# Kernel optimization log

Hardware: AMD Instinct MI355X
Metric: run time of the kernel (lower is better)

The kernel has to match this reference:

```python
import jax, jax.numpy as jnp
import numpy as np

N = 65536       # num nodes
F = 128         # num_features
D = 256         # embedding_dim
E = N * 8       # num edges
CS = 32         # target_cluster_size
DEPTH = 8
H = 8
NCLS = 10


def setup_inputs() -> dict:
    key = jax.random.key(0)
    ks = jax.random.split(key, 16)
    r = lambda k, shp: (jax.random.normal(k, shp, jnp.float32) * 0.02)
    return {
        "x": jax.random.normal(ks[0], (N, F), jnp.float32),
        "edge_index": jax.random.randint(ks[1], (2, E), 0, N),
        "W_in": r(ks[2], (F, D)), "b_in": jnp.zeros((D,), jnp.float32),
        "W_gat": r(ks[3], (D, D)), "a_src": r(ks[4], (D,)), "a_dst": r(ks[5], (D,)),
        "b_gat": jnp.zeros((D,), jnp.float32),
        "W_emb": r(ks[6], (CS * D, D)), "b_emb": jnp.zeros((D,), jnp.float32),
        "class_tok": r(ks[7], (D,)),
        "ln1_s": jnp.ones((DEPTH, D), jnp.float32), "ln1_b": jnp.zeros((DEPTH, D), jnp.float32),
        "Wqkv": r(ks[8], (DEPTH, D, 3 * D)), "bqkv": jnp.zeros((DEPTH, 3 * D), jnp.float32),
        "Wproj": r(ks[9], (DEPTH, D, D)), "bproj": jnp.zeros((DEPTH, D), jnp.float32),
        "ln2_s": jnp.ones((DEPTH, D), jnp.float32), "ln2_b": jnp.zeros((DEPTH, D), jnp.float32),
        "W1": r(ks[10], (DEPTH, D, 4 * D)), "b1": jnp.zeros((DEPTH, 4 * D), jnp.float32),
        "W2": r(ks[11], (DEPTH, 4 * D, D)), "b2": jnp.zeros((DEPTH, D), jnp.float32),
        "W_cls": r(ks[12], (D, NCLS)), "b_cls": jnp.zeros((NCLS,), jnp.float32),
    }


def _layernorm(x, s, b):
    m = jnp.mean(x, -1, keepdims=True)
    v = jnp.var(x, -1, keepdims=True)
    return (x - m) * jax.lax.rsqrt(v + 1e-5) * s + b


def _forward(x, edge_index, W_in, b_in, W_gat, a_src, a_dst, b_gat, W_emb, b_emb,
             class_tok, ln1_s, ln1_b, Wqkv, bqkv, Wproj, bproj, ln2_s, ln2_b,
             W1, b1, W2, b2, W_cls, b_cls):
    # input_layer: LazyLinear(F -> D)
    h = x @ W_in + b_in                                   # [N, D]
    # GATConv(D -> D), 1 head, add_self_loops=True
    loop = jnp.arange(N)
    src = jnp.concatenate([edge_index[0], loop])          # message source j
    dst = jnp.concatenate([edge_index[1], loop])          # message target i
    Wh = h @ W_gat                                        # [N, D]
    e = jax.nn.leaky_relu((Wh @ a_src)[src] + (Wh @ a_dst)[dst], 0.2)
    emax = jax.ops.segment_max(e, dst, num_segments=N)
    ee = jnp.exp(e - emax[dst])
    denom = jax.ops.segment_sum(ee, dst, num_segments=N)
    alpha = ee / denom[dst]                               # softmax over incoming edges
    h = jax.ops.segment_sum(alpha[:, None] * Wh[src], dst, num_segments=N) + b_gat
    # clusters of 32 contiguous nodes: gather, flatten, embeddings_layer (32*D -> D)
    tok = h.reshape(N // CS, CS * D) @ W_emb + b_emb      # [num_clusters, D]
    seq = jnp.concatenate([class_tok[None, :], tok])[None]  # [1, S, D], S = num_clusters + 1
    scale = (D // H) ** -0.5
    for i in range(DEPTH):
        y = _layernorm(seq, ln1_s[i], ln1_b[i])
        qkv = (y @ Wqkv[i] + bqkv[i]).reshape(1, -1, 3, H, D // H)
        q, k, v = qkv[:, :, 0], qkv[:, :, 1], qkv[:, :, 2]
        att = jax.nn.softmax(jnp.einsum('bshd,bthd->bhst', q, k) * scale, axis=-1)
        o = jnp.einsum('bhst,bthd->bshd', att, v).reshape(1, -1, D)
        seq = seq + (o @ Wproj[i] + bproj[i])
        y = _layernorm(seq, ln2_s[i], ln2_b[i])
        seq = seq + (jax.nn.gelu(y @ W1[i] + b1[i], approximate=False) @ W2[i] + b2[i])
    # to_class on the class token
    return seq[0, 0][None, :] @ W_cls + b_cls             # [1, NCLS]


def reference(x, edge_index, W_in, b_in, W_gat, a_src, a_dst, b_gat, W_emb, b_emb,
              class_tok, ln1_s, ln1_b, Wqkv, bqkv, Wproj, bproj, ln2_s, ln2_b,
              W1, b1, W2, b2, W_cls, b_cls):
    return _forward(x, edge_index, W_in, b_in, W_gat, a_src, a_dst, b_gat, W_emb,
                    b_emb, class_tok, ln1_s, ln1_b, Wqkv, bqkv, Wproj, bproj,
                    ln2_s, ln2_b, W1, b1, W2, b2, W_cls, b_cls)
```

## Files before the change

### kernel.cpp

```cpp
#include <hip/hip_runtime.h>
#include <math.h>

#define N_NODES 65536
#define F_IN 128
#define D_MODEL 256
#define E_EDGES 524288
#define EE_EDGES 589824
#define SEQ_LEN 2049
#define SEQ_PAD 2112
#define NHEAD 8
#define HDIM 32
#define NCLS 10
#define NSPLIT 4

typedef unsigned short u16;
typedef __attribute__((ext_vector_type(8))) short s8v;
typedef __attribute__((ext_vector_type(4))) float f4v;

__device__ __forceinline__ u16 f2bf(float f)
{
    union { float f; unsigned u; } v; v.f = f;
    unsigned r = v.u + 0x7FFF + ((v.u >> 16) & 1);
    return (u16)(r >> 16);
}
__device__ __forceinline__ float bf2f(u16 h)
{
    union { unsigned u; float f; } v; v.u = ((unsigned)h) << 16;
    return v.f;
}

__global__ __launch_bounds__(256) void prep_weight(
    const float* __restrict__ W, u16* __restrict__ Oh, u16* __restrict__ Ol,
    int K, int N, long long strideW, long long strideO, int write_lo)
{
    const float* Wz = W + (size_t)blockIdx.z * strideW;
    u16* Ohz = Oh + (size_t)blockIdx.z * strideO;
    u16* Olz = Ol + (size_t)blockIdx.z * strideO;
    __shared__ u16 th[64][68];
    __shared__ u16 tl[64][68];
    int kb = blockIdx.x * 64, nb = blockIdx.y * 64;
    int t = threadIdx.x;
    int kr = t >> 4, nc = (t & 15) * 4;
#pragma unroll
    for (int i = 0; i < 4; ++i) {
        int k = kr + i * 16;
        float4 v = *(const float4*)(Wz + (size_t)(kb + k) * N + nb + nc);
        float vv[4] = {v.x, v.y, v.z, v.w};
#pragma unroll
        for (int e = 0; e < 4; ++e) {
            u16 h = f2bf(vv[e]);
            th[k][nc + e] = h;
            if (write_lo) tl[k][nc + e] = f2bf(vv[e] - bf2f(h));
        }
    }
    __syncthreads();
    int nr = t >> 4, kc = (t & 15) * 4;
#pragma unroll
    for (int i = 0; i < 4; ++i) {
        int n = nr + i * 16;
        uint2 oh;
        oh.x = (unsigned)th[kc + 0][n] | ((unsigned)th[kc + 1][n] << 16);
        oh.y = (unsigned)th[kc + 2][n] | ((unsigned)th[kc + 3][n] << 16);
        *(uint2*)(Ohz + (size_t)(nb + n) * K + kb + kc) = oh;
        if (write_lo) {
            uint2 ol;
            ol.x = (unsigned)tl[kc + 0][n] | ((unsigned)tl[kc + 1][n] << 16);
            ol.y = (unsigned)tl[kc + 2][n] | ((unsigned)tl[kc + 3][n] << 16);
            *(uint2*)(Olz + (size_t)(nb + n) * K + kb + kc) = ol;
        }
    }
}

template<int ACT, int RES, int ATOM, int OB, int APRE, int TERMS, int FATT>
__global__ __launch_bounds__(256) void hgemm(
    const void* __restrict__ A, const u16* __restrict__ Al2,
    const u16* __restrict__ Bh, const u16* __restrict__ Bl,
    const float* __restrict__ bias, const float* __restrict__ Rsd,
    float* __restrict__ C, const float* __restrict__ Mp,
    const float* __restrict__ Lp,
    int M, int N, int K, int Kc)
{
    __shared__ __align__(16) u16 SS[(TERMS == 3 ? 4 : 2) * 2048];
    u16* const AhS = SS;
    u16* const BhS = SS + 2048;
    u16* const AlS = SS + 4096;
    u16* const BlS = SS + 6144;
    const int tid = threadIdx.x;
    const int bn = blockIdx.x * 64, bm = blockIdx.y * 64;
    const int kb = blockIdx.z * Kc;
    const int r = tid >> 2, cch = tid & 3;
    const int widx = r * 32 + ((cch ^ ((r >> 1) & 3)) << 3);
    const int w = tid >> 6, lane = tid & 63;
    const int wm = w >> 1, wn = w & 1;
    const int lr = lane & 15, lc = lane >> 4;
    const int ar0 = wm * 32 + lr, ar1 = ar0 + 16;
    const int nr0 = wn * 32 + lr, nr1 = nr0 + 16;
    const int ai0 = ar0 * 32 + ((lc ^ ((ar0 >> 1) & 3)) << 3);
    const int ai1 = ar1 * 32 + ((lc ^ ((ar1 >> 1) & 3)) << 3);
    const int bi0 = nr0 * 32 + ((lc ^ ((nr0 >> 1) & 3)) << 3);
    const int bi1 = nr1 * 32 + ((lc ^ ((nr1 >> 1) & 3)) << 3);

    f4v acc00 = {0.f, 0.f, 0.f, 0.f}, acc01 = acc00, acc10 = acc00, acc11 = acc00;

    const int gr = bm + r;
    const float* apf = (const float*)A + (size_t)gr * K + kb + cch * 8;
    const u16*   aph = (const u16*)A + (size_t)gr * K + kb + cch * 8;
    const u16*   apl = Al2 ? Al2 + (size_t)gr * K + kb + cch * 8 : (const u16*)0;
    const u16* bhp = Bh + (size_t)(bn + r) * K + kb + cch * 8;
    const u16* blp = (TERMS == 3) ? Bl + (size_t)(bn + r) * K + kb + cch * 8
                                  : (const u16*)0;

    float fac_s[FATT ? NSPLIT : 1][FATT ? 2 : 1];
    float invL[FATT ? 2 : 1];
    if (FATT) {
        if (gr < M) {
#pragma unroll
            for (int hh = 0; hh < 2; ++hh) {
                int h = (kb >> 5) + hh;
                float ms[NSPLIT], ls[NSPLIT], Mx = -1e30f;
#pragma unroll
                for (int s = 0; s < NSPLIT; ++s) {
                    ms[s] = Mp[((size_t)s * SEQ_PAD + gr) * NHEAD + h];
                    ls[s] = Lp[((size_t)s * SEQ_PAD + gr) * NHEAD + h];
                    Mx = fmaxf(Mx, ms[s]);
                }
                float L = 0.f;
#pragma unroll
                for (int s = 0; s < NSPLIT; ++s) {
                    float f = __expf(ms[s] - Mx);
                    fac_s[s][hh] = f;
                    L += ls[s] * f;
                }
                invL[hh] = 1.f / L;
            }
        } else {
#pragma unroll
            for (int hh = 0; hh < 2; ++hh) {
                invL[hh] = 0.f;
#pragma unroll
                for (int s = 0; s < NSPLIT; ++s) fac_s[s][hh] = 0.f;
            }
        }
    }

    for (int k0 = 0; k0 < Kc; k0 += 32) {
        s8v hv = {0, 0, 0, 0, 0, 0, 0, 0}, lv = hv;
        if (FATT) {
            if (gr < M) {
                int hh = k0 >> 5;
                float v[8] = {0.f, 0.f, 0.f, 0.f, 0.f, 0.f, 0.f, 0.f};
#pragma unroll
                for (int s = 0; s < NSPLIT; ++s) {
                    const float* op = (const float*)A
                        + ((size_t)s * SEQ_PAD + gr) * 256 + kb + k0 + cch * 8;
                    float4 x0 = *(const float4*)op;
                    float4 x1 = *(const float4*)(op + 4);
                    float f = fac_s[s][hh];
                    v[0] += f * x0.x; v[1] += f * x0.y;
                    v[2] += f * x0.z; v[3] += f * x0.w;
                    v[4] += f * x1.x; v[5] += f * x1.y;
                    v[6] += f * x1.z; v[7] += f * x1.w;
                }
                float il = invL[hh];
#pragma unroll
                for (int e = 0; e < 8; ++e) hv[e] = (short)f2bf(v[e] * il);
            }
        } else if (APRE) {
            if (gr < M) {
                hv = *(const s8v*)aph;
                if (TERMS == 3) lv = *(const s8v*)apl;
            }
        } else {
            float v[8] = {0.f, 0.f, 0.f, 0.f, 0.f, 0.f, 0.f, 0.f};
            if (gr < M) {
                float4 x0 = *(const float4*)apf;
                float4 x1 = *(const float4*)(apf + 4);
                v[0] = x0.x; v[1] = x0.y; v[2] = x0.z; v[3] = x0.w;
                v[4] = x1.x; v[5] = x1.y; v[6] = x1.z; v[7] = x1.w;
            }
#pragma unroll
            for (int e = 0; e < 8; ++e) {
                u16 h = f2bf(v[e]);
                hv[e] = (short)h;
                if (TERMS == 3) lv[e] = (short)f2bf(v[e] - bf2f(h));
            }
        }
        *(s8v*)&AhS[widx] = hv;
        *(s8v*)&BhS[widx] = *(const s8v*)bhp;
        if (TERMS == 3) {
            *(s8v*)&AlS[widx] = lv;
            *(s8v*)&BlS[widx] = *(const s8v*)blp;
        }
        __syncthreads();

        s8v a0h = *(s8v*)&AhS[ai0], a1h = *(s8v*)&AhS[ai1];
        s8v b0h = *(s8v*)&BhS[bi0], b1h = *(s8v*)&BhS[bi1];
        acc00 = __builtin_amdgcn_mfma_f32_16x16x32_bf16(a0h, b0h, acc00, 0, 0, 0);
        acc01 = __builtin_amdgcn_mfma_f32_16x16x32_bf16(a0h, b1h, acc01, 0, 0, 0);
        acc10 = __builtin_amdgcn_mfma_f32_16x16x32_bf16(a1h, b0h, acc10, 0, 0, 0);
        acc11 = __builtin_amdgcn_mfma_f32_16x16x32_bf16(a1h, b1h, acc11, 0, 0, 0);
        if (TERMS == 3) {
            s8v a0l = *(s8v*)&AlS[ai0], a1l = *(s8v*)&AlS[ai1];
            s8v b0l = *(s8v*)&BlS[bi0], b1l = *(s8v*)&BlS[bi1];
            acc00 = __builtin_amdgcn_mfma_f32_16x16x32_bf16(a0h, b0l, acc00, 0, 0, 0);
            acc00 = __builtin_amdgcn_mfma_f32_16x16x32_bf16(a0l, b0h, acc00, 0, 0, 0);
            acc01 = __builtin_amdgcn_mfma_f32_16x16x32_bf16(a0h, b1l, acc01, 0, 0, 0);
            acc01 = __builtin_amdgcn_mfma_f32_16x16x32_bf16(a0l, b1h, acc01, 0, 0, 0);
            acc10 = __builtin_amdgcn_mfma_f32_16x16x32_bf16(a1h, b0l, acc10, 0, 0, 0);
            acc10 = __builtin_amdgcn_mfma_f32_16x16x32_bf16(a1l, b0h, acc10, 0, 0, 0);
            acc11 = __builtin_amdgcn_mfma_f32_16x16x32_bf16(a1h, b1l, acc11, 0, 0, 0);
            acc11 = __builtin_amdgcn_mfma_f32_16x16x32_bf16(a1l, b1h, acc11, 0, 0, 0);
        }
        __syncthreads();
        apf += 32; aph += 32; if (TERMS == 3) apl += 32;
        bhp += 32; if (TERMS == 3) blp += 32;
    }

#pragma unroll
    for (int fg = 0; fg < 4; ++fg) {
        int f = fg >> 1, g = fg & 1;
        f4v a = (fg == 0) ? acc00 : (fg == 1) ? acc01 : (fg == 2) ? acc10 : acc11;
        int col = bn + wn * 32 + g * 16 + lr;
        int row0 = bm + wm * 32 + f * 16 + lc * 4;
#pragma unroll
        for (int j = 0; j < 4; ++j) {
            int rr = row0 + j;
            if (rr < M) {
                float vv = a[j];
                if (ATOM) {
                    atomicAdd(&C[(size_t)rr * N + col], vv);
                } else {
                    if (bias) vv += bias[col];
                    if (ACT == 1) vv = 0.5f * vv * (1.0f + erff(vv * 0.70710678118654752f));
                    if (RES) vv += Rsd[(size_t)rr * N + col];
                    if (OB == 1) ((u16*)C)[(size_t)rr * N + col] = f2bf(vv);
                    else         C[(size_t)rr * N + col] = vv;
                }
            }
        }
    }
}

__global__ void init_seq(float* __restrict__ seq, const float* __restrict__ bias,
                         const float* __restrict__ cls)
{
    int row = blockIdx.x;
    int t = threadIdx.x;
    seq[(size_t)row * 256 + t] = (row == 0) ? cls[t] : bias[t];
}

__global__ void pad_zero_u32(unsigned* __restrict__ p, int n)
{
    int i = blockIdx.x * 256 + threadIdx.x;
    if (i < n) p[i] = 0u;
}

__global__ void vecmat256(const float* __restrict__ v, const float* __restrict__ W,
                          float* __restrict__ out)
{
    int n = threadIdx.x;
    float acc = 0.f;
    for (int k = 0; k < 256; ++k) acc += v[k] * W[k * 256 + n];
    out[n] = acc;
}

__global__ void gat_init(float* __restrict__ emax, float* __restrict__ denom,
                         int* __restrict__ deg)
{
    int i = blockIdx.x * 256 + threadIdx.x;
    emax[i] = -1e30f;
    denom[i] = 0.f;
    deg[i] = 0;
}

__global__ __launch_bounds__(256) void gat_scores(
    const u16* __restrict__ WH, const float* __restrict__ a_src,
    const float* __restrict__ a_dst, float* __restrict__ s_src,
    float* __restrict__ s_dst)
{
    int gid = blockIdx.x * 256 + threadIdx.x;
    int node = gid >> 6;
    int lane = gid & 63;
    uint2 rv = *(const uint2*)(WH + (size_t)node * D_MODEL + (lane << 2));
    float d0 = __uint_as_float(rv.x << 16);
    float d1 = __uint_as_float(rv.x & 0xffff0000u);
    float d2 = __uint_as_float(rv.y << 16);
    float d3 = __uint_as_float(rv.y & 0xffff0000u);
    float4 asv = *(const float4*)(a_src + (lane << 2));
    float4 adv = *(const float4*)(a_dst + (lane << 2));
    float as = d0 * asv.x + d1 * asv.y + d2 * asv.z + d3 * asv.w;
    float ad = d0 * adv.x + d1 * adv.y + d2 * adv.z + d3 * adv.w;
#pragma unroll
    for (int off = 32; off; off >>= 1) {
        as += __shfl_down(as, off);
        ad += __shfl_down(ad, off);
    }
    if (lane == 0) { s_src[node] = as; s_dst[node] = ad; }
}

__device__ __forceinline__ void atomicMaxFloat(float* addr, float val)
{
    int* ai = (int*)addr;
    int old = __float_as_int(*addr);
    while (__int_as_float(old) < val) {
        int prev = atomicCAS(ai, old, __float_as_int(val));
        if (prev == old) break;
        old = prev;
    }
}

__global__ void edge_pass1(const int* __restrict__ ei, const float* __restrict__ s_src,
                           const float* __restrict__ s_dst, float* __restrict__ e_buf,
                           float* __restrict__ emax, int* __restrict__ deg)
{
    int j = blockIdx.x * 256 + threadIdx.x;
    if (j >= EE_EDGES) return;
    int s, d;
    if (j < E_EDGES) { s = ei[j]; d = ei[E_EDGES + j]; }
    else { s = d = j - E_EDGES; }
    float e = s_src[s] + s_dst[d];
    e = (e > 0.f) ? e : 0.2f * e;
    e_buf[j] = e;
    atomicMaxFloat(&emax[d], e);
    atomicAdd(&deg[d], 1);
}

__global__ void scan1(const int* __restrict__ in, int* __restrict__ out_excl,
                      int* __restrict__ bsum)
{
    __shared__ int s[256];
    int t = threadIdx.x;
    int i = blockIdx.x * 256 + t;
    int v = in[i];
    s[t] = v;
    __syncthreads();
    for (int off = 1; off < 256; off <<= 1) {
        int u = (t >= off) ? s[t - off] : 0;
        __syncthreads();
        s[t] += u;
        __syncthreads();
    }
    out_excl[i] = s[t] - v;
    if (t == 255) bsum[blockIdx.x] = s[255];
}

__global__ void scan2(int* __restrict__ bsum)
{
    __shared__ int s[256];
    int t = threadIdx.x;
    int v = bsum[t];
    s[t] = v;
    __syncthreads();
    for (int off = 1; off < 256; off <<= 1) {
        int u = (t >= off) ? s[t - off] : 0;
        __syncthreads();
        s[t] += u;
        __syncthreads();
    }
    bsum[t] = s[t] - v;
}

__global__ void scan3(int* __restrict__ offs, const int* __restrict__ bsum,
                      int* __restrict__ cur)
{
    int i = blockIdx.x * 256 + threadIdx.x;
    int v = offs[i] + bsum[blockIdx.x];
    offs[i] = v;
    cur[i] = v;
}

__global__ void edge_pass2(const int* __restrict__ ei, const float* __restrict__ e_buf,
                           const float* __restrict__ emax, float* __restrict__ denom,
                           int* __restrict__ cur, int* __restrict__ csr_src,
                           float* __restrict__ csr_w)
{
    int j = blockIdx.x * 256 + threadIdx.x;
    if (j >= EE_EDGES) return;
    int s, d;
    if (j < E_EDGES) { s = ei[j]; d = ei[E_EDGES + j]; }
    else { s = d = j - E_EDGES; }
    float ee = __expf(e_buf[j] - emax[d]);
    atomicAdd(&denom[d], ee);
    int pos = atomicAdd(&cur[d], 1);
    csr_src[pos] = s;
    csr_w[pos] = ee;
}

__global__ __launch_bounds__(256) void gat_aggregate(
    const u16* __restrict__ WH, const int* __restrict__ csr_src,
    const float* __restrict__ csr_w, const int* __restrict__ offs,
    const int* __restrict__ deg, const float* __restrict__ denom,
    const float* __restrict__ b_gat, u16* __restrict__ hH)
{
    int gid = blockIdx.x * 256 + threadIdx.x;
    int node = gid >> 6;
    int lane = gid & 63;
    float inv = 1.0f / denom[node];
    float a0 = 0.f, a1 = 0.f, a2 = 0.f, a3 = 0.f;
    int s0 = offs[node], e0 = s0 + deg[node];
    for (int k = s0; k < e0; ++k) {
        int src = csr_src[k];
        float alpha = csr_w[k] * inv;
        uint2 rv = *(const uint2*)(WH + (size_t)src * D_MODEL + (lane << 2));
        a0 += alpha * __uint_as_float(rv.x << 16);
        a1 += alpha * __uint_as_float(rv.x & 0xffff0000u);
        a2 += alpha * __uint_as_float(rv.y << 16);
        a3 += alpha * __uint_as_float(rv.y & 0xffff0000u);
    }
    float4 bg = *(const float4*)(b_gat + (lane << 2));
    float v0 = a0 + bg.x, v1 = a1 + bg.y, v2 = a2 + bg.z, v3 = a3 + bg.w;
    uint2 ho;
    ho.x = (unsigned)f2bf(v0) | ((unsigned)f2bf(v1) << 16);
    ho.y = (unsigned)f2bf(v2) | ((unsigned)f2bf(v3) << 16);
    *(uint2*)(hH + (size_t)node * D_MODEL + (lane << 2)) = ho;
}

__global__ __launch_bounds__(256) void ln_kernel(
    float* __restrict__ seqio, const float* __restrict__ sc,
    const float* __restrict__ bi, u16* __restrict__ Yh,
    const float* __restrict__ badd)
{
    int row = blockIdx.x;
    int t = threadIdx.x;
    float x = seqio[(size_t)row * 256 + t];
    float sum = x, sq = x * x;
#pragma unroll
    for (int off = 32; off; off >>= 1) {
        sum += __shfl_down(sum, off);
        sq  += __shfl_down(sq, off);
    }
    __shared__ float rs[4], rq[4];
    if ((t & 63) == 0) { rs[t >> 6] = sum; rq[t >> 6] = sq; }
    __syncthreads();
    sum = rs[0] + rs[1] + rs[2] + rs[3];
    sq  = rq[0] + rq[1] + rq[2] + rq[3];
    float mean = sum * (1.f / 256.f);
    float var  = sq * (1.f / 256.f) - mean * mean;
    float r = rsqrtf(var + 1e-5f);
    float y = (x - mean) * r * sc[t] + bi[t];
    Yh[(size_t)row * 256 + t] = f2bf(y);
    seqio[(size_t)row * 256 + t] = x + badd[t];
}

__global__ __launch_bounds__(256) void mfma_attn_split(
    const u16* __restrict__ QKV, float* __restrict__ Opart,
    float* __restrict__ Mpart, float* __restrict__ Lpart)
{
    __shared__ __align__(16) u16 Ks[64 * 32];
    __shared__ __align__(16) u16 Vt[32 * 72];
    __shared__ __align__(16) u16 Ps[4 * 16 * 72];
    const int tid = threadIdx.x;
    const int w = tid >> 6, lane = tid & 63;
    const int g = lane >> 4, ql = lane & 15;
    const int h = blockIdx.y;
    const int sp = blockIdx.z;
    const int t0 = (33 * sp) / NSPLIT, t1 = (33 * (sp + 1)) / NSPLIT;
    const int qbase = blockIdx.x * 64 + w * 16;
    const float scale = 0.17677669529663687f;

    int qrow = qbase + ql; if (qrow > SEQ_LEN - 1) qrow = SEQ_LEN - 1;
    const s8v qfrag = *(const s8v*)(QKV + (size_t)qrow * 768 + h * 32 + g * 8);

    f4v o0 = {0.f, 0.f, 0.f, 0.f}, o1 = o0;
    float m[4], l[4];
#pragma unroll
    for (int r = 0; r < 4; ++r) { m[r] = -1e30f; l[r] = 0.f; }

    const int sr = tid >> 2, sc_ = tid & 3;
    const int kslot = sc_ ^ ((sr >> 1) & 3);
    u16* const psw = &Ps[w * 1152];

    for (int t = t0; t < t1; ++t) {
        __syncthreads();
        {
            int grow = t * 64 + sr;
            const u16* kp = QKV + (size_t)grow * 768 + 256 + h * 32 + sc_ * 8;
            s8v kvv = *(const s8v*)kp;
            s8v vvv = *(const s8v*)(kp + 256);
            *(s8v*)&Ks[sr * 32 + kslot * 8] = kvv;
#pragma unroll
            for (int e = 0; e < 8; ++e) Vt[(sc_ * 8 + e) * 72 + sr] = (u16)vvv[e];
        }
        __syncthreads();

        f4v s[4];
        const f4v zz = {0.f, 0.f, 0.f, 0.f};
#pragma unroll
        for (int c = 0; c < 4; ++c) {
            int kvloc = c * 16 + ql;
            s8v kf = *(s8v*)&Ks[kvloc * 32 + ((g ^ ((kvloc >> 1) & 3)) << 3)];
            s[c] = __builtin_amdgcn_mfma_f32_16x16x32_bf16(qfrag, kf, zz, 0, 0, 0);
            int kvg = t * 64 + kvloc;
            bool valid = (kvg < SEQ_LEN);
#pragma unroll
            for (int r = 0; r < 4; ++r)
                s[c][r] = valid ? s[c][r] * scale : -1e30f;
        }

        float mloc[4];
#pragma unroll
        for (int r = 0; r < 4; ++r) {
            float v = fmaxf(fmaxf(s[0][r], s[1][r]), fmaxf(s[2][r], s[3][r]));
            v = fmaxf(v, __shfl_xor(v, 1));
            v = fmaxf(v, __shfl_xor(v, 2));
            v = fmaxf(v, __shfl_xor(v, 4));
            v = fmaxf(v, __shfl_xor(v, 8));
            mloc[r] = v;
        }
        float fac[4];
#pragma unroll
        for (int r = 0; r < 4; ++r) {
            float mn = fmaxf(m[r], mloc[r]);
            fac[r] = __expf(m[r] - mn);
            m[r] = mn;
        }
#pragma unroll
        for (int c = 0; c < 4; ++c)
#pragma unroll
            for (int r = 0; r < 4; ++r)
                s[c][r] = __expf(s[c][r] - m[r]);
#pragma unroll
        for (int r = 0; r < 4; ++r) {
            float ls = s[0][r] + s[1][r] + s[2][r] + s[3][r];
            ls += __shfl_xor(ls, 1);
            ls += __shfl_xor(ls, 2);
            ls += __shfl_xor(ls, 4);
            ls += __shfl_xor(ls, 8);
            l[r] = l[r] * fac[r] + ls;
            o0[r] *= fac[r];
            o1[r] *= fac[r];
        }

#pragma unroll
        for (int c = 0; c < 4; ++c)
#pragma unroll
            for (int r = 0; r < 4; ++r)
                psw[(g * 4 + r) * 72 + c * 16 + ql] = f2bf(s[c][r]);

#pragma unroll
        for (int kch = 0; kch < 2; ++kch) {
            s8v pf = *(s8v*)&psw[ql * 72 + kch * 32 + g * 8];
            s8v v0 = *(s8v*)&Vt[ql * 72 + kch * 32 + g * 8];
            s8v v1 = *(s8v*)&Vt[(16 + ql) * 72 + kch * 32 + g * 8];
            o0 = __builtin_amdgcn_mfma_f32_16x16x32_bf16(pf, v0, o0, 0, 0, 0);
            o1 = __builtin_amdgcn_mfma_f32_16x16x32_bf16(pf, v1, o1, 0, 0, 0);
        }
    }

#pragma unroll
    for (int r = 0; r < 4; ++r) {
        int q = qbase + g * 4 + r;
        if (q < SEQ_LEN) {
            size_t base = ((size_t)sp * SEQ_PAD + q) * 256 + h * 32;
            Opart[base + ql] = o0[r];
            Opart[base + 16 + ql] = o1[r];
            if (ql == 0) {
                Mpart[((size_t)sp * SEQ_PAD + q) * NHEAD + h] = m[r];
                Lpart[((size_t)sp * SEQ_PAD + q) * NHEAD + h] = l[r];
            }
        }
    }
}

__global__ void cls_head(const float* __restrict__ seq, const float* __restrict__ W,
                         const float* __restrict__ b, float* __restrict__ out)
{
    __shared__ float s[256];
    int t = threadIdx.x;
    s[t] = seq[t];
    __syncthreads();
    if (t < NCLS) {
        float acc = b[t];
        for (int k = 0; k < 256; ++k) acc += s[k] * W[k * NCLS + t];
        out[t] = acc;
    }
}

extern "C" void kernel_launch(void* const* d_in, const int* in_sizes, int n_in,
                              void* d_out, int out_size, void* d_ws, size_t ws_size,
                              hipStream_t stream)
{
    (void)in_sizes; (void)n_in; (void)out_size; (void)ws_size;
    const float* x       = (const float*)d_in[0];
    const int*   ei      = (const int*)d_in[1];
    const float* W_in    = (const float*)d_in[2];
    const float* b_in    = (const float*)d_in[3];
    const float* W_gat   = (const float*)d_in[4];
    const float* a_src   = (const float*)d_in[5];
    const float* a_dst   = (const float*)d_in[6];
    const float* b_gat   = (const float*)d_in[7];
    const float* W_emb   = (const float*)d_in[8];
    const float* b_emb   = (const float*)d_in[9];
    const float* cls_tok = (const float*)d_in[10];
    const float* ln1_s   = (const float*)d_in[11];
    const float* ln1_b   = (const float*)d_in[12];
    const float* Wqkv    = (const float*)d_in[13];
    const float* bqkv    = (const float*)d_in[14];
    const float* Wproj   = (const float*)d_in[15];
    const float* bproj   = (const float*)d_in[16];
    const float* ln2_s   = (const float*)d_in[17];
    const float* ln2_b   = (const float*)d_in[18];
    const float* W1      = (const float*)d_in[19];
    const float* b1      = (const float*)d_in[20];
    const float* W2      = (const float*)d_in[21];
    const float* b2      = (const float*)d_in[22];
    const float* W_cls   = (const float*)d_in[23];
    const float* b_cls   = (const float*)d_in[24];
    float* out = (float*)d_out;

    float* ws = (float*)d_ws;
    u16*   bufWHu = (u16*)ws;
    float* seqb  = ws;
    u16*   Yh    = (u16*)(ws + 524544);
    u16*   QKVb  = (u16*)(ws + 1049088);
    u16*   MLPHh = (u16*)(ws + 2384640);
    u16*   wreg  = (u16*)(ws + 5500000);
    u16* embh  = wreg;
    u16* embl  = wreg + 2097152;
    u16* qkvh  = wreg + 4194304;
    u16* qkvl  = wreg + 5767168;
    u16* projh = wreg + 7340032;
    u16* projl = wreg + 7864320;
    u16* w1h   = wreg + 8388608;
    u16* w1l   = wreg + 10485760;
    u16* w2h   = wreg + 12582912;
    u16* w2l   = wreg + 14680064;
    u16*   hH    = (u16*)(ws + 16777216);
    float* Opart = ws + 16777216;
    float* Mpart = Opart + (size_t)NSPLIT * SEQ_PAD * 256;
    float* Lpart = Mpart + (size_t)NSPLIT * SEQ_PAD * NHEAD;
    float* sm    = ws + 2 * 16777216;
    float* s_src = sm;
    float* s_dst = sm + 65536;
    float* emaxb = sm + 2 * 65536;
    float* denom = sm + 3 * 65536;
    float* e_buf = sm + 4 * 65536;
    float* csr_w = e_buf + 589824;
    float* Wc    = csr_w + 589824;
    float* bc    = Wc + 32768;
    int*   deg     = (int*)(bc + 256);
    int*   offs    = deg + 65536;
    int*   cur     = offs + 65536;
    int*   bsum    = cur + 65536;
    int*   csr_src = bsum + 256;
    u16*   wgTh = (u16*)(csr_src + 589824);
    u16*   wgTl = wgTh + 65536;
    u16*   wcTh = wgTh + 131072;
    u16*   wcTl = wcTh + 32768;

    gat_init<<<256, 256, 0, stream>>>(emaxb, denom, deg);
    prep_weight<<<dim3(4, 4, 1), 256, 0, stream>>>(W_gat, wgTh, wgTl, 256, 256,
                                                   0, 0, 1);
    hgemm<0,0,0,0,0,3,0><<<dim3(4, 2, 1), 256, 0, stream>>>(
        W_in, nullptr, wgTh, wgTl, nullptr, nullptr, Wc, nullptr, nullptr,
        128, 256, 256, 256);
    vecmat256<<<1, 256, 0, stream>>>(b_in, W_gat, bc);
    prep_weight<<<dim3(2, 4, 1), 256, 0, stream>>>(Wc, wcTh, wcTl, 128, 256,
                                                   0, 0, 0);
    hgemm<0,0,0,1,0,1,0><<<dim3(4, 1024, 1), 256, 0, stream>>>(
        x, nullptr, wcTh, nullptr, bc, nullptr, (float*)bufWHu, nullptr, nullptr,
        N_NODES, 256, 128, 128);
    gat_scores<<<16384, 256, 0, stream>>>(bufWHu, a_src, a_dst, s_src, s_dst);
    edge_pass1<<<EE_EDGES / 256, 256, 0, stream>>>(ei, s_src, s_dst, e_buf, emaxb, deg);
    scan1<<<256, 256, 0, stream>>>(deg, offs, bsum);
    scan2<<<1, 256, 0, stream>>>(bsum);
    scan3<<<256, 256, 0, stream>>>(offs, bsum, cur);
    edge_pass2<<<EE_EDGES / 256, 256, 0, stream>>>(ei, e_buf, emaxb, denom, cur,
                                                   csr_src, csr_w);
    gat_aggregate<<<16384, 256, 0, stream>>>(bufWHu, csr_src, csr_w, offs, deg,
                                             denom, b_gat, hH);

    prep_weight<<<dim3(128, 4, 1), 256, 0, stream>>>(W_emb, embh, embl, 8192, 256,
                                                     0, 0, 0);
    prep_weight<<<dim3(4, 12, 8), 256, 0, stream>>>(Wqkv, qkvh, qkvl, 256, 768,
                                                    196608, 196608, 0);
    prep_weight<<<dim3(4, 4, 8), 256, 0, stream>>>(Wproj, projh, projl, 256, 256,
                                                   65536, 65536, 0);
    prep_weight<<<dim3(4, 16, 8), 256, 0, stream>>>(W1, w1h, w1l, 256, 1024,
                                                    262144, 262144, 0);
    prep_weight<<<dim3(16, 4, 8), 256, 0, stream>>>(W2, w2h, w2l, 1024, 256,
                                                    262144, 262144, 0);

    init_seq<<<SEQ_LEN, 256, 0, stream>>>(seqb, b_emb, cls_tok);
    hgemm<0,0,1,0,1,1,0><<<dim3(4, 32, 8), 256, 0, stream>>>(
        (const void*)hH, nullptr, embh, nullptr, nullptr, nullptr, seqb + 256,
        nullptr, nullptr, 2048, 256, 8192, 1024);

    pad_zero_u32<<<95, 256, 0, stream>>>(
        (unsigned*)(QKVb + (size_t)SEQ_LEN * 768), (SEQ_PAD - SEQ_LEN) * 768 / 2);

    for (int i = 0; i < 8; ++i) {
        ln_kernel<<<SEQ_LEN, 256, 0, stream>>>(seqb, ln1_s + i * 256,
                                               ln1_b + i * 256, Yh,
                                               bproj + i * 256);
        hgemm<0,0,0,1,1,1,0><<<dim3(12, 33, 1), 256, 0, stream>>>(
            (const void*)Yh, nullptr, qkvh + (size_t)i * 196608, nullptr,
            bqkv + i * 768, nullptr, (float*)QKVb, nullptr, nullptr,
            SEQ_LEN, 768, 256, 256);
        mfma_attn_split<<<dim3(33, NHEAD, NSPLIT), 256, 0, stream>>>(
            QKVb, Opart, Mpart, Lpart);
        hgemm<0,0,1,0,0,1,1><<<dim3(4, 33, 4), 256, 0, stream>>>(
            (const void*)Opart, nullptr, projh + (size_t)i * 65536, nullptr,
            nullptr, nullptr, seqb, Mpart, Lpart, SEQ_LEN, 256, 256, 64);
        ln_kernel<<<SEQ_LEN, 256, 0, stream>>>(seqb, ln2_s + i * 256,
                                               ln2_b + i * 256, Yh,
                                               b2 + i * 256);
        hgemm<1,0,0,1,1,1,0><<<dim3(16, 33, 1), 256, 0, stream>>>(
            (const void*)Yh, nullptr, w1h + (size_t)i * 262144, nullptr,
            b1 + i * 1024, nullptr, (float*)MLPHh, nullptr, nullptr,
            SEQ_LEN, 1024, 256, 256);
        hgemm<0,0,1,0,1,1,0><<<dim3(4, 33, 4), 256, 0, stream>>>(
            (const void*)MLPHh, nullptr, w2h + (size_t)i * 262144, nullptr,
            nullptr, nullptr, seqb, nullptr, nullptr, SEQ_LEN, 256, 1024, 256);
    }

    cls_head<<<1, 256, 0, stream>>>(seqb, W_cls, b_cls, out);
}
```

Before: 1.054 ms.

## Fold LayerNorm affine into weights and normalize inside GEMM A-load

LayerNorm scale is folded into the QKV and W1 weights during weight prep, and the LN bias is folded into precomputed GEMM biases. A light per-row stats kernel replaces the full LN kernel, and the GEMM normalizes fp32 rows on the fly while converting to bf16. The residual bias adds move into the atomic GEMM epilogues, applied by the first K-split only. GAT aggregation is also unrolled by four with normalization deferred to the end. This removes the bf16 Yh round trip, at the cost of fp32 A loads and slightly different rounding.

```diff
diff --git a/kernel.cpp b/kernel.cpp
--- a/kernel.cpp
+++ b/kernel.cpp
@@ -31,11 +31,13 @@
 
 __global__ __launch_bounds__(256) void prep_weight(
     const float* __restrict__ W, u16* __restrict__ Oh, u16* __restrict__ Ol,
-    int K, int N, long long strideW, long long strideO, int write_lo)
+    int K, int N, long long strideW, long long strideO, int write_lo,
+    const float* __restrict__ scale)
 {
     const float* Wz = W + (size_t)blockIdx.z * strideW;
     u16* Ohz = Oh + (size_t)blockIdx.z * strideO;
     u16* Olz = Ol + (size_t)blockIdx.z * strideO;
+    const float* scz = scale ? scale + (size_t)blockIdx.z * D_MODEL : nullptr;
     __shared__ u16 th[64][68];
     __shared__ u16 tl[64][68];
     int kb = blockIdx.x * 64, nb = blockIdx.y * 64;
@@ -44,8 +46,9 @@
 #pragma unroll
     for (int i = 0; i < 4; ++i) {
         int k = kr + i * 16;
+        float sv = scz ? scz[kb + k] : 1.f;
         float4 v = *(const float4*)(Wz + (size_t)(kb + k) * N + nb + nc);
-        float vv[4] = {v.x, v.y, v.z, v.w};
+        float vv[4] = {v.x * sv, v.y * sv, v.z * sv, v.w * sv};
 #pragma unroll
         for (int e = 0; e < 4; ++e) {
             u16 h = f2bf(vv[e]);
@@ -71,7 +74,43 @@
     }
 }
 
-template<int ACT, int RES, int ATOM, int OB, int APRE, int TERMS, int FATT>
+__global__ void bias_fold(const float* __restrict__ lnb, const float* __restrict__ W,
+                          const float* __restrict__ b0, float* __restrict__ out,
+                          int N, long long strideW)
+{
+    int z = blockIdx.y;
+    int n = blockIdx.x * 256 + threadIdx.x;
+    if (n >= N) return;
+    const float* Wz = W + (size_t)z * strideW;
+    const float* lz = lnb + (size_t)z * D_MODEL;
+    float acc = b0[(size_t)z * N + n];
+    for (int k = 0; k < D_MODEL; ++k) acc += lz[k] * Wz[(size_t)k * N + n];
+    out[(size_t)z * N + n] = acc;
+}
+
+__global__ __launch_bounds__(256) void ln_stats(
+    const float* __restrict__ seq, float* __restrict__ mu, float* __restrict__ rs)
+{
+    int row = blockIdx.x * 4 + (threadIdx.x >> 6);
+    int lane = threadIdx.x & 63;
+    if (row >= SEQ_LEN) return;
+    float4 v = *(const float4*)(seq + (size_t)row * 256 + (lane << 2));
+    float s1 = v.x + v.y + v.z + v.w;
+    float s2 = v.x * v.x + v.y * v.y + v.z * v.z + v.w * v.w;
+#pragma unroll
+    for (int off = 32; off; off >>= 1) {
+        s1 += __shfl_xor(s1, off);
+        s2 += __shfl_xor(s2, off);
+    }
+    if (lane == 0) {
+        float m = s1 * (1.f / 256.f);
+        float var = s2 * (1.f / 256.f) - m * m;
+        mu[row] = m;
+        rs[row] = rsqrtf(var + 1e-5f);
+    }
+}
+
+template<int ACT, int RES, int ATOM, int OB, int APRE, int TERMS, int FATT, int LNS>
 __global__ __launch_bounds__(256) void hgemm(
     const void* __restrict__ A, const u16* __restrict__ Al2,
     const u16* __restrict__ Bh, const u16* __restrict__ Bl,
@@ -110,6 +149,11 @@
     const u16* blp = (TERMS == 3) ? Bl + (size_t)(bn + r) * K + kb + cch * 8
                                   : (const u16*)0;
 
+    float mu_r = 0.f, rs_r = 1.f;
+    if (LNS) {
+        if (gr < M) { mu_r = Mp[gr]; rs_r = Lp[gr]; }
+    }
+
     float fac_s[FATT ? NSPLIT : 1][FATT ? 2 : 1];
     float invL[FATT ? 2 : 1];
     if (FATT) {
@@ -180,9 +224,10 @@
             }
 #pragma unroll
             for (int e = 0; e < 8; ++e) {
-                u16 h = f2bf(v[e]);
+                float vv = LNS ? (v[e] - mu_r) * rs_r : v[e];
+                u16 h = f2bf(vv);
                 hv[e] = (short)h;
-                if (TERMS == 3) lv[e] = (short)f2bf(v[e] - bf2f(h));
+                if (TERMS == 3) lv[e] = (short)f2bf(vv - bf2f(h));
             }
         }
         *(s8v*)&AhS[widx] = hv;
@@ -228,6 +273,7 @@
             if (rr < M) {
                 float vv = a[j];
                 if (ATOM) {
+                    if (bias && blockIdx.z == 0) vv += bias[col];
                     atomicAdd(&C[(size_t)rr * N + col], vv);
                 } else {
                     if (bias) vv += bias[col];
@@ -395,51 +441,44 @@
     int gid = blockIdx.x * 256 + threadIdx.x;
     int node = gid >> 6;
     int lane = gid & 63;
-    float inv = 1.0f / denom[node];
     float a0 = 0.f, a1 = 0.f, a2 = 0.f, a3 = 0.f;
     int s0 = offs[node], e0 = s0 + deg[node];
-    for (int k = s0; k < e0; ++k) {
+    int k = s0;
+    for (; k + 4 <= e0; k += 4) {
+        int i0 = csr_src[k], i1 = csr_src[k + 1];
+        int i2 = csr_src[k + 2], i3 = csr_src[k + 3];
+        float w0 = csr_w[k], w1 = csr_w[k + 1];
+        float w2 = csr_w[k + 2], w3 = csr_w[k + 3];
+        uint2 r0 = *(const uint2*)(WH + (size_t)i0 * D_MODEL + (lane << 2));
+        uint2 r1 = *(const uint2*)(WH + (size_t)i1 * D_MODEL + (lane << 2));
+        uint2 r2 = *(const uint2*)(WH + (size_t)i2 * D_MODEL + (lane << 2));
+        uint2 r3 = *(const uint2*)(WH + (size_t)i3 * D_MODEL + (lane << 2));
+        a0 += w0 * __uint_as_float(r0.x << 16) + w1 * __uint_as_float(r1.x << 16)
+            + w2 * __uint_as_float(r2.x << 16) + w3 * __uint_as_float(r3.x << 16);
+        a1 += w0 * __uint_as_float(r0.x & 0xffff0000u) + w1 * __uint_as_float(r1.x & 0xffff0000u)
+            + w2 * __uint_as_float(r2.x & 0xffff0000u) + w3 * __uint_as_float(r3.x & 0xffff0000u);
+        a2 += w0 * __uint_as_float(r0.y << 16) + w1 * __uint_as_float(r1.y << 16)
+            + w2 * __uint_as_float(r2.y << 16) + w3 * __uint_as_float(r3.y << 16);
+        a3 += w0 * __uint_as_float(r0.y & 0xffff0000u) + w1 * __uint_as_float(r1.y & 0xffff0000u)
+            + w2 * __uint_as_float(r2.y & 0xffff0000u) + w3 * __uint_as_float(r3.y & 0xffff0000u);
+    }
+    for (; k < e0; ++k) {
         int src = csr_src[k];
-        float alpha = csr_w[k] * inv;
+        float alpha = csr_w[k];
         uint2 rv = *(const uint2*)(WH + (size_t)src * D_MODEL + (lane << 2));
         a0 += alpha * __uint_as_float(rv.x << 16);
         a1 += alpha * __uint_as_float(rv.x & 0xffff0000u);
         a2 += alpha * __uint_as_float(rv.y << 16);
         a3 += alpha * __uint_as_float(rv.y & 0xffff0000u);
     }
+    float inv = 1.0f / denom[node];
     float4 bg = *(const float4*)(b_gat + (lane << 2));
-    float v0 = a0 + bg.x, v1 = a1 + bg.y, v2 = a2 + bg.z, v3 = a3 + bg.w;
+    float v0 = a0 * inv + bg.x, v1 = a1 * inv + bg.y;
+    float v2 = a2 * inv + bg.z, v3 = a3 * inv + bg.w;
     uint2 ho;
     ho.x = (unsigned)f2bf(v0) | ((unsigned)f2bf(v1) << 16);
     ho.y = (unsigned)f2bf(v2) | ((unsigned)f2bf(v3) << 16);
     *(uint2*)(hH + (size_t)node * D_MODEL + (lane << 2)) = ho;
-}
-
-__global__ __launch_bounds__(256) void ln_kernel(
-    float* __restrict__ seqio, const float* __restrict__ sc,
-    const float* __restrict__ bi, u16* __restrict__ Yh,
-    const float* __restrict__ badd)
-{
-    int row = blockIdx.x;
-    int t = threadIdx.x;
-    float x = seqio[(size_t)row * 256 + t];
-    float sum = x, sq = x * x;
-#pragma unroll
-    for (int off = 32; off; off >>= 1) {
-        sum += __shfl_down(sum, off);
-        sq  += __shfl_down(sq, off);
-    }
-    __shared__ float rs[4], rq[4];
-    if ((t & 63) == 0) { rs[t >> 6] = sum; rq[t >> 6] = sq; }
-    __syncthreads();
-    sum = rs[0] + rs[1] + rs[2] + rs[3];
-    sq  = rq[0] + rq[1] + rq[2] + rq[3];
-    float mean = sum * (1.f / 256.f);
-    float var  = sq * (1.f / 256.f) - mean * mean;
-    float r = rsqrtf(var + 1e-5f);
-    float y = (x - mean) * r * sc[t] + bi[t];
-    Yh[(size_t)row * 256 + t] = f2bf(y);
-    seqio[(size_t)row * 256 + t] = x + badd[t];
 }
 
 __global__ __launch_bounds__(256) void mfma_attn_split(
@@ -611,9 +650,12 @@
     float* ws = (float*)d_ws;
     u16*   bufWHu = (u16*)ws;
     float* seqb  = ws;
-    u16*   Yh    = (u16*)(ws + 524544);
     u16*   QKVb  = (u16*)(ws + 1049088);
     u16*   MLPHh = (u16*)(ws + 2384640);
+    float* qkvBias = ws + 3500000;
+    float* w1Bias  = qkvBias + 8 * 768;
+    float* muA     = w1Bias + 8 * 1024;
+    float* rsA     = muA + 2112;
     u16*   wreg  = (u16*)(ws + 5500000);
     u16* embh  = wreg;
     u16* embl  = wreg + 2097152;
@@ -650,14 +692,14 @@
 
     gat_init<<<256, 256, 0, stream>>>(emaxb, denom, deg);
     prep_weight<<<dim3(4, 4, 1), 256, 0, stream>>>(W_gat, wgTh, wgTl, 256, 256,
-                                                   0, 0, 1);
-    hgemm<0,0,0,0,0,3,0><<<dim3(4, 2, 1), 256, 0, stream>>>(
+                                                   0, 0, 1, nullptr);
+    hgemm<0,0,0,0,0,3,0,0><<<dim3(4, 2, 1), 256, 0, stream>>>(
         W_in, nullptr, wgTh, wgTl, nullptr, nullptr, Wc, nullptr, nullptr,
         128, 256, 256, 256);
     vecmat256<<<1, 256, 0, stream>>>(b_in, W_gat, bc);
     prep_weight<<<dim3(2, 4, 1), 256, 0, stream>>>(Wc, wcTh, wcTl, 128, 256,
-                                                   0, 0, 0);
-    hgemm<0,0,0,1,0,1,0><<<dim3(4, 1024, 1), 256, 0, stream>>>(
+                                                   0, 0, 0, nullptr);
+    hgemm<0,0,0,1,0,1,0,0><<<dim3(4, 1024, 1), 256, 0, stream>>>(
         x, nullptr, wcTh, nullptr, bc, nullptr, (float*)bufWHu, nullptr, nullptr,
         N_NODES, 256, 128, 128);
     gat_scores<<<16384, 256, 0, stream>>>(bufWHu, a_src, a_dst, s_src, s_dst);
@@ -671,18 +713,20 @@
                                              denom, b_gat, hH);
 
     prep_weight<<<dim3(128, 4, 1), 256, 0, stream>>>(W_emb, embh, embl, 8192, 256,
-                                                     0, 0, 0);
+                                                     0, 0, 0, nullptr);
     prep_weight<<<dim3(4, 12, 8), 256, 0, stream>>>(Wqkv, qkvh, qkvl, 256, 768,
-                                                    196608, 196608, 0);
+                                                    196608, 196608, 0, ln1_s);
     prep_weight<<<dim3(4, 4, 8), 256, 0, stream>>>(Wproj, projh, projl, 256, 256,
-                                                   65536, 65536, 0);
+                                                   65536, 65536, 0, nullptr);
     prep_weight<<<dim3(4, 16, 8), 256, 0, stream>>>(W1, w1h, w1l, 256, 1024,
-                                                    262144, 262144, 0);
+                                                    262144, 262144, 0, ln2_s);
     prep_weight<<<dim3(16, 4, 8), 256, 0, stream>>>(W2, w2h, w2l, 1024, 256,
-                                                    262144, 262144, 0);
+                                                    262144, 262144, 0, nullptr);
+    bias_fold<<<dim3(3, 8), 256, 0, stream>>>(ln1_b, Wqkv, bqkv, qkvBias, 768, 196608);
+    bias_fold<<<dim3(4, 8), 256, 0, stream>>>(ln2_b, W1, b1, w1Bias, 1024, 262144);
 
     init_seq<<<SEQ_LEN, 256, 0, stream>>>(seqb, b_emb, cls_tok);
-    hgemm<0,0,1,0,1,1,0><<<dim3(4, 32, 8), 256, 0, stream>>>(
+    hgemm<0,0,1,0,1,1,0,0><<<dim3(4, 32, 8), 256, 0, stream>>>(
         (const void*)hH, nullptr, embh, nullptr, nullptr, nullptr, seqb + 256,
         nullptr, nullptr, 2048, 256, 8192, 1024);
 
@@ -690,28 +734,26 @@
         (unsigned*)(QKVb + (size_t)SEQ_LEN * 768), (SEQ_PAD - SEQ_LEN) * 768 / 2);
 
     for (int i = 0; i < 8; ++i) {
-        ln_kernel<<<SEQ_LEN, 256, 0, stream>>>(seqb, ln1_s + i * 256,
-                                               ln1_b + i * 256, Yh,
-                                               bproj + i * 256);
-        hgemm<0,0,0,1,1,1,0><<<dim3(12, 33, 1), 256, 0, stream>>>(
-            (const void*)Yh, nullptr, qkvh + (size_t)i * 196608, nullptr,
-            bqkv + i * 768, nullptr, (float*)QKVb, nullptr, nullptr,
+        ln_stats<<<513, 256, 0, stream>>>(seqb, muA, rsA);
+        hgemm<0,0,0,1,0,1,0,1><<<dim3(12, 33, 1), 256, 0, stream>>>(
+            (const void*)seqb, nullptr, qkvh + (size_t)i * 196608, nullptr,
+            qkvBias + (size_t)i * 768, nullptr, (float*)QKVb, muA, rsA,
             SEQ_LEN, 768, 256, 256);
         mfma_attn_split<<<dim3(33, NHEAD, NSPLIT), 256, 0, stream>>>(
             QKVb, Opart, Mpart, Lpart);
-        hgemm<0,0,1,0,0,1,1><<<dim3(4, 33, 4), 256, 0, stream>>>(
+        hgemm<0,0,1,0,0,1,1,0><<<dim3(4, 33, 4), 256, 0, stream>>>(
             (const void*)Opart, nullptr, projh + (size_t)i * 65536, nullptr,
-            nullptr, nullptr, seqb, Mpart, Lpart, SEQ_LEN, 256, 256, 64);
-        ln_kernel<<<SEQ_LEN, 256, 0, stream>>>(seqb, ln2_s + i * 256,
-                                               ln2_b + i * 256, Yh,
-                                               b2 + i * 256);
-        hgemm<1,0,0,1,1,1,0><<<dim3(16, 33, 1), 256, 0, stream>>>(
-            (const void*)Yh, nullptr, w1h + (size_t)i * 262144, nullptr,
-            b1 + i * 1024, nullptr, (float*)MLPHh, nullptr, nullptr,
+            bproj + (size_t)i * 256, nullptr, seqb, Mpart, Lpart,
+            SEQ_LEN, 256, 256, 64);
+        ln_stats<<<513, 256, 0, stream>>>(seqb, muA, rsA);
+        hgemm<1,0,0,1,0,1,0,1><<<dim3(16, 33, 1), 256, 0, stream>>>(
+            (const void*)seqb, nullptr, w1h + (size_t)i * 262144, nullptr,
+            w1Bias + (size_t)i * 1024, nullptr, (float*)MLPHh, muA, rsA,
             SEQ_LEN, 1024, 256, 256);
-        hgemm<0,0,1,0,1,1,0><<<dim3(4, 33, 4), 256, 0, stream>>>(
+        hgemm<0,0,1,0,1,1,0,0><<<dim3(4, 33, 4), 256, 0, stream>>>(
             (const void*)MLPHh, nullptr, w2h + (size_t)i * 262144, nullptr,
-            nullptr, nullptr, seqb, nullptr, nullptr, SEQ_LEN, 256, 1024, 256);
+            b2 + (size_t)i * 256, nullptr, seqb, nullptr, nullptr,
+            SEQ_LEN, 256, 1024, 256);
     }
 
     cls_head<<<1, 256, 0, stream>>>(seqb, W_cls, b_cls, out);
```

After: 1.122 ms. 1.07x slower.

## Drop per-node max in GAT softmax and unroll edge aggregation by four

Applied to the files above, without the earlier changes.

Removes the per-destination max reduction (CAS-based atomic max) and the atomic denominator accumulation. Raw exp(e) weights are now stored in the CSR and normalised by their sum inside the aggregate kernel. The aggregation loop is unrolled four-wide so several neighbour row loads are in flight at once. Skipping max subtraction risks overflow if scores grow large, but attention scores here are small.

```diff
diff --git a/kernel.cpp b/kernel.cpp
--- a/kernel.cpp
+++ b/kernel.cpp
@@ -264,12 +264,9 @@
     out[n] = acc;
 }
 
-__global__ void gat_init(float* __restrict__ emax, float* __restrict__ denom,
-                         int* __restrict__ deg)
+__global__ void gat_init(int* __restrict__ deg)
 {
     int i = blockIdx.x * 256 + threadIdx.x;
-    emax[i] = -1e30f;
-    denom[i] = 0.f;
     deg[i] = 0;
 }
 
@@ -298,30 +295,11 @@
     if (lane == 0) { s_src[node] = as; s_dst[node] = ad; }
 }
 
-__device__ __forceinline__ void atomicMaxFloat(float* addr, float val)
-{
-    int* ai = (int*)addr;
-    int old = __float_as_int(*addr);
-    while (__int_as_float(old) < val) {
-        int prev = atomicCAS(ai, old, __float_as_int(val));
-        if (prev == old) break;
-        old = prev;
-    }
-}
-
-__global__ void edge_pass1(const int* __restrict__ ei, const float* __restrict__ s_src,
-                           const float* __restrict__ s_dst, float* __restrict__ e_buf,
-                           float* __restrict__ emax, int* __restrict__ deg)
+__global__ void edge_deg(const int* __restrict__ ei, int* __restrict__ deg)
 {
     int j = blockIdx.x * 256 + threadIdx.x;
     if (j >= EE_EDGES) return;
-    int s, d;
-    if (j < E_EDGES) { s = ei[j]; d = ei[E_EDGES + j]; }
-    else { s = d = j - E_EDGES; }
-    float e = s_src[s] + s_dst[d];
-    e = (e > 0.f) ? e : 0.2f * e;
-    e_buf[j] = e;
-    atomicMaxFloat(&emax[d], e);
+    int d = (j < E_EDGES) ? ei[E_EDGES + j] : j - E_EDGES;
     atomicAdd(&deg[d], 1);
 }
 
@@ -369,46 +347,67 @@
     cur[i] = v;
 }
 
-__global__ void edge_pass2(const int* __restrict__ ei, const float* __restrict__ e_buf,
-                           const float* __restrict__ emax, float* __restrict__ denom,
-                           int* __restrict__ cur, int* __restrict__ csr_src,
-                           float* __restrict__ csr_w)
+__global__ void edge_fill(const int* __restrict__ ei, const float* __restrict__ s_src,
+                          const float* __restrict__ s_dst, int* __restrict__ cur,
+                          int* __restrict__ csr_src, float* __restrict__ csr_w)
 {
     int j = blockIdx.x * 256 + threadIdx.x;
     if (j >= EE_EDGES) return;
     int s, d;
     if (j < E_EDGES) { s = ei[j]; d = ei[E_EDGES + j]; }
     else { s = d = j - E_EDGES; }
-    float ee = __expf(e_buf[j] - emax[d]);
-    atomicAdd(&denom[d], ee);
+    float e = s_src[s] + s_dst[d];
+    e = (e > 0.f) ? e : 0.2f * e;
     int pos = atomicAdd(&cur[d], 1);
     csr_src[pos] = s;
-    csr_w[pos] = ee;
+    csr_w[pos] = __expf(e);
 }
 
 __global__ __launch_bounds__(256) void gat_aggregate(
     const u16* __restrict__ WH, const int* __restrict__ csr_src,
     const float* __restrict__ csr_w, const int* __restrict__ offs,
-    const int* __restrict__ deg, const float* __restrict__ denom,
-    const float* __restrict__ b_gat, u16* __restrict__ hH)
+    const int* __restrict__ deg, const float* __restrict__ b_gat,
+    u16* __restrict__ hH)
 {
     int gid = blockIdx.x * 256 + threadIdx.x;
     int node = gid >> 6;
     int lane = gid & 63;
-    float inv = 1.0f / denom[node];
-    float a0 = 0.f, a1 = 0.f, a2 = 0.f, a3 = 0.f;
+    float a0 = 0.f, a1 = 0.f, a2 = 0.f, a3 = 0.f, wsum = 0.f;
     int s0 = offs[node], e0 = s0 + deg[node];
-    for (int k = s0; k < e0; ++k) {
+    int k = s0;
+    for (; k + 4 <= e0; k += 4) {
+        int i0 = csr_src[k], i1 = csr_src[k + 1];
+        int i2 = csr_src[k + 2], i3 = csr_src[k + 3];
+        float w0 = csr_w[k], w1 = csr_w[k + 1];
+        float w2 = csr_w[k + 2], w3 = csr_w[k + 3];
+        uint2 r0 = *(const uint2*)(WH + (size_t)i0 * D_MODEL + (lane << 2));
+        uint2 r1 = *(const uint2*)(WH + (size_t)i1 * D_MODEL + (lane << 2));
+        uint2 r2 = *(const uint2*)(WH + (size_t)i2 * D_MODEL + (lane << 2));
+        uint2 r3 = *(const uint2*)(WH + (size_t)i3 * D_MODEL + (lane << 2));
+        wsum += (w0 + w1) + (w2 + w3);
+        a0 += w0 * __uint_as_float(r0.x << 16) + w1 * __uint_as_float(r1.x << 16)
+            + w2 * __uint_as_float(r2.x << 16) + w3 * __uint_as_float(r3.x << 16);
+        a1 += w0 * __uint_as_float(r0.x & 0xffff0000u) + w1 * __uint_as_float(r1.x & 0xffff0000u)
+            + w2 * __uint_as_float(r2.x & 0xffff0000u) + w3 * __uint_as_float(r3.x & 0xffff0000u);
+        a2 += w0 * __uint_as_float(r0.y << 16) + w1 * __uint_as_float(r1.y << 16)
+            + w2 * __uint_as_float(r2.y << 16) + w3 * __uint_as_float(r3.y << 16);
+        a3 += w0 * __uint_as_float(r0.y & 0xffff0000u) + w1 * __uint_as_float(r1.y & 0xffff0000u)
+            + w2 * __uint_as_float(r2.y & 0xffff0000u) + w3 * __uint_as_float(r3.y & 0xffff0000u);
+    }
+    for (; k < e0; ++k) {
         int src = csr_src[k];
-        float alpha = csr_w[k] * inv;
+        float alpha = csr_w[k];
         uint2 rv = *(const uint2*)(WH + (size_t)src * D_MODEL + (lane << 2));
+        wsum += alpha;
         a0 += alpha * __uint_as_float(rv.x << 16);
         a1 += alpha * __uint_as_float(rv.x & 0xffff0000u);
         a2 += alpha * __uint_as_float(rv.y << 16);
         a3 += alpha * __uint_as_float(rv.y & 0xffff0000u);
     }
+    float inv = 1.0f / wsum;
     float4 bg = *(const float4*)(b_gat + (lane << 2));
-    float v0 = a0 + bg.x, v1 = a1 + bg.y, v2 = a2 + bg.z, v3 = a3 + bg.w;
+    float v0 = a0 * inv + bg.x, v1 = a1 * inv + bg.y;
+    float v2 = a2 * inv + bg.z, v3 = a3 * inv + bg.w;
     uint2 ho;
     ho.x = (unsigned)f2bf(v0) | ((unsigned)f2bf(v1) << 16);
     ho.y = (unsigned)f2bf(v2) | ((unsigned)f2bf(v3) << 16);
@@ -632,10 +631,7 @@
     float* sm    = ws + 2 * 16777216;
     float* s_src = sm;
     float* s_dst = sm + 65536;
-    float* emaxb = sm + 2 * 65536;
-    float* denom = sm + 3 * 65536;
-    float* e_buf = sm + 4 * 65536;
-    float* csr_w = e_buf + 589824;
+    float* csr_w = sm + 2 * 65536;
     float* Wc    = csr_w + 589824;
     float* bc    = Wc + 32768;
     int*   deg     = (int*)(bc + 256);
@@ -648,7 +644,7 @@
     u16*   wcTh = wgTh + 131072;
     u16*   wcTl = wcTh + 32768;
 
-    gat_init<<<256, 256, 0, stream>>>(emaxb, denom, deg);
+    gat_init<<<256, 256, 0, stream>>>(deg);
     prep_weight<<<dim3(4, 4, 1), 256, 0, stream>>>(W_gat, wgTh, wgTl, 256, 256,
                                                    0, 0, 1);
     hgemm<0,0,0,0,0,3,0><<<dim3(4, 2, 1), 256, 0, stream>>>(
@@ -661,14 +657,14 @@
         x, nullptr, wcTh, nullptr, bc, nullptr, (float*)bufWHu, nullptr, nullptr,
         N_NODES, 256, 128, 128);
     gat_scores<<<16384, 256, 0, stream>>>(bufWHu, a_src, a_dst, s_src, s_dst);
-    edge_pass1<<<EE_EDGES / 256, 256, 0, stream>>>(ei, s_src, s_dst, e_buf, emaxb, deg);
+    edge_deg<<<EE_EDGES / 256, 256, 0, stream>>>(ei, deg);
     scan1<<<256, 256, 0, stream>>>(deg, offs, bsum);
     scan2<<<1, 256, 0, stream>>>(bsum);
     scan3<<<256, 256, 0, stream>>>(offs, bsum, cur);
-    edge_pass2<<<EE_EDGES / 256, 256, 0, stream>>>(ei, e_buf, emaxb, denom, cur,
-                                                   csr_src, csr_w);
+    edge_fill<<<EE_EDGES / 256, 256, 0, stream>>>(ei, s_src, s_dst, cur,
+                                                  csr_src, csr_w);
     gat_aggregate<<<16384, 256, 0, stream>>>(bufWHu, csr_src, csr_w, offs, deg,
-                                             denom, b_gat, hH);
+                                             b_gat, hH);
 
     prep_weight<<<dim3(128, 4, 1), 256, 0, stream>>>(W_emb, embh, embl, 8192, 256,
                                                      0, 0, 0);
```

Result: faster. 960.1 us (-8.9%).
